# Kernel optimization log

Hardware: AMD Instinct MI355X
Metric: run time of the kernel (lower is better)

The kernel has to match this reference:

```python
import jax, jax.numpy as jnp
import numpy as np

D_MODEL = 1024
D_INNER = 2048   # expand * d_model
D_STATE = 16
D_CONV = 4
DT_RANK = 64     # ceil(d_model / 16)
BATCH = 4
SEQLEN = 2048


def _dw_causal_conv(x, w, b):
    # x: (B, d, L); w: (d, 1, K) depthwise; causal left pad K-1 -> output length L
    y = jax.lax.conv_general_dilated(
        x, w, window_strides=(1,), padding=[(D_CONV - 1, 0)],
        dimension_numbers=("NCH", "OIH", "NCH"), feature_group_count=x.shape[1])
    return y + b[None, :, None]


def _ssm_pass(x_conv, z, A_log, x_proj_w, dt_proj_w, dt_proj_b, D):
    # x_conv, z: (B, d, L)
    Bsz, d, L = x_conv.shape
    u = jax.nn.silu(x_conv)                                   # (B, d, L)
    x_dbl = jnp.einsum("bdl,rd->blr", u, x_proj_w)            # (B, L, dt_rank+2N)
    dt = x_dbl[..., :DT_RANK]
    Bm = x_dbl[..., DT_RANK:DT_RANK + D_STATE]                # (B, L, N)
    Cm = x_dbl[..., DT_RANK + D_STATE:]                       # (B, L, N)
    delta = jax.nn.softplus(jnp.einsum("blr,dr->bld", dt, dt_proj_w) + dt_proj_b)  # (B, L, d)
    A = -jnp.exp(A_log)                                       # (d, N)

    # time-major inputs for scan
    delta_t = jnp.transpose(delta, (1, 0, 2))                 # (L, B, d)
    u_t = jnp.transpose(u, (2, 0, 1))                         # (L, B, d)
    Bm_t = jnp.transpose(Bm, (1, 0, 2))                       # (L, B, N)
    Cm_t = jnp.transpose(Cm, (1, 0, 2))                       # (L, B, N)

    def step(h, inp):
        d_s, B_s, C_s, u_s = inp                              # (B,d) (B,N) (B,N) (B,d)
        dA = jnp.exp(d_s[:, :, None] * A)                     # (B, d, N)
        h = dA * h + (d_s * u_s)[:, :, None] * B_s[:, None, :]
        y = jnp.einsum("bdn,bn->bd", h, C_s)
        return h, y

    h0 = jnp.zeros((Bsz, d, D_STATE), dtype=u.dtype)
    _, ys = jax.lax.scan(step, h0, (delta_t, Bm_t, Cm_t, u_t))  # ys: (L, B, d)
    y = jnp.transpose(ys, (1, 2, 0)) + D[None, :, None] * u     # (B, d, L)
    return y * jax.nn.silu(z)


def setup_inputs() -> dict:
    key = jax.random.key(0)
    ks = jax.random.split(key, 16)
    s = 0.02
    hidden_states = jax.random.normal(ks[0], (BATCH, SEQLEN, D_MODEL), jnp.float32)
    in_proj_w = jax.random.normal(ks[1], (2 * D_INNER, D_MODEL), jnp.float32) * s
    conv_w_f = jax.random.normal(ks[2], (D_INNER, 1, D_CONV), jnp.float32) * 0.2
    conv_b_f = jax.random.normal(ks[3], (D_INNER,), jnp.float32) * 0.1
    conv_w_b = jax.random.normal(ks[4], (D_INNER, 1, D_CONV), jnp.float32) * 0.2
    conv_b_b = jax.random.normal(ks[5], (D_INNER,), jnp.float32) * 0.1
    x_proj_w_f = jax.random.normal(ks[6], (DT_RANK + 2 * D_STATE, D_INNER), jnp.float32) * s
    dt_proj_w_f = jax.random.uniform(ks[7], (D_INNER, DT_RANK), jnp.float32, -DT_RANK**-0.5, DT_RANK**-0.5)
    x_proj_w_b = jax.random.normal(ks[8], (DT_RANK + 2 * D_STATE, D_INNER), jnp.float32) * s
    dt_proj_w_b = jax.random.uniform(ks[9], (D_INNER, DT_RANK), jnp.float32, -DT_RANK**-0.5, DT_RANK**-0.5)
    # dt bias init: inverse-softplus of dt sampled log-uniform in [1e-3, 1e-1]
    dt = jnp.exp(jax.random.uniform(ks[10], (D_INNER,)) * (np.log(0.1) - np.log(0.001)) + np.log(0.001))
    dt = jnp.clip(dt, 1e-4, None)
    inv_dt = dt + jnp.log(-jnp.expm1(-dt))
    dt_proj_b_f = inv_dt
    dt_proj_b_b = inv_dt
    A_log = jnp.log(jnp.broadcast_to(jnp.arange(1, D_STATE + 1, dtype=jnp.float32), (D_INNER, D_STATE)))
    out_proj_w = jax.random.normal(ks[11], (D_MODEL, D_INNER), jnp.float32) * s
    return {
        "hidden_states": hidden_states, "in_proj_w": in_proj_w,
        "conv_w_f": conv_w_f, "conv_b_f": conv_b_f, "conv_w_b": conv_w_b, "conv_b_b": conv_b_b,
        "x_proj_w_f": x_proj_w_f, "dt_proj_w_f": dt_proj_w_f, "dt_proj_b_f": dt_proj_b_f,
        "x_proj_w_b": x_proj_w_b, "dt_proj_w_b": dt_proj_w_b, "dt_proj_b_b": dt_proj_b_b,
        "A_log_f": A_log, "A_log_b": A_log,
        "D_f": jnp.ones((D_INNER,), jnp.float32), "D_b": jnp.ones((D_INNER,), jnp.float32),
        "out_proj_w": out_proj_w,
    }


def reference(hidden_states, in_proj_w, conv_w_f, conv_b_f, conv_w_b, conv_b_b,
              x_proj_w_f, dt_proj_w_f, dt_proj_b_f, x_proj_w_b, dt_proj_w_b, dt_proj_b_b,
              A_log_f, A_log_b, D_f, D_b, out_proj_w):
    L = hidden_states.shape[1]
    xz = jnp.einsum("bld,ed->bel", hidden_states, in_proj_w)  # (B, 2*d_inner, L)
    x, z = xz[:, :D_INNER], xz[:, D_INNER:]

    # forward direction
    x_conv_f = _dw_causal_conv(x, conv_w_f, conv_b_f)[..., :L]
    y_f = _ssm_pass(x_conv_f, z, A_log_f, x_proj_w_f, dt_proj_w_f, dt_proj_b_f, D_f)

    # backward direction
    x_b, z_b = x[..., ::-1], z[..., ::-1]
    x_conv_b = _dw_causal_conv(x_b, conv_w_b, conv_b_b)[..., :L]
    y_b = _ssm_pass(x_conv_b, z_b, A_log_b, x_proj_w_b, dt_proj_w_b, dt_proj_b_b, D_b)[..., ::-1]

    y = (y_f + y_b) / 2.0                                     # if_divide_out=True
    out = jnp.einsum("bdl,ed->ble", y, out_proj_w)            # (B, L, d_model)
    return out
```

## Files before the change

### kernel.cpp

```cpp
#include <hip/hip_runtime.h>


#define Bsz  4
#define LSEQ 2048
#define DM   1024
#define DI   2048
#define DS   16
#define MROWS (Bsz * LSEQ)
#define NCH  32
#define CLEN 64

typedef unsigned short u16b;
typedef __attribute__((ext_vector_type(8))) short short8;
typedef __attribute__((ext_vector_type(4))) float f32x4;
typedef __attribute__((address_space(3))) unsigned int lds_u32;
typedef const __attribute__((address_space(1))) unsigned int glb_u32;

__device__ __forceinline__ float b2f(u16b u) {
  union { unsigned int i; float f; } x; x.i = ((unsigned int)u) << 16; return x.f;
}
__device__ __forceinline__ u16b f2b(float f) {
  union { float f; unsigned int i; } x; x.f = f;
  unsigned int r = x.i + 0x7FFFu + ((x.i >> 16) & 1u);
  return (u16b)(r >> 16);
}
__device__ __forceinline__ u16b f2b_cvt(float f) {
  unsigned int r;
  asm("v_cvt_pk_bf16_f32 %0, %1, %1" : "=v"(r) : "v"(f));
  return (u16b)r;
}
__device__ __forceinline__ float fast_rcp(float x) {
  return __builtin_amdgcn_rcpf(x);
}
__device__ __forceinline__ float softplus_fast(float v) {
  float e = __expf(-fabsf(v));
  return fmaxf(v, 0.f) + __logf(1.f + e);
}
__device__ __forceinline__ void pow_ladder(float q, float* dA) {
  float q2 = q * q, q3 = q2 * q, q4 = q2 * q2;
  float q5 = q4 * q, q6 = q4 * q2, q7 = q4 * q3, q8 = q4 * q4;
  dA[0] = q;  dA[1] = q2;  dA[2] = q3;  dA[3] = q4;
  dA[4] = q5; dA[5] = q6;  dA[6] = q7;  dA[7] = q8;
  dA[8] = q8 * q;  dA[9] = q8 * q2;  dA[10] = q8 * q3;  dA[11] = q8 * q4;
  dA[12] = q8 * q5; dA[13] = q8 * q6; dA[14] = q8 * q7; dA[15] = q8 * q8;
}

__device__ __forceinline__ int xcd_swz(int id, int nwg) {
  int c = nwg >> 3;
  return (id & 7) * c + (id >> 3);
}

__device__ __forceinline__ void stage_tile(const u16b* gbase, int ld,
                                           u16b* lds, int wave, int lane) {
#pragma unroll
  for (int t = 0; t < 4; ++t) {
    int rb = wave * 32 + t * 8;
    int r = rb + (lane >> 3);
    int cb = (lane & 7) ^ (r & 7);
    const u16b* g = gbase + (size_t)r * ld + cb * 8;
    __builtin_amdgcn_global_load_lds((glb_u32*)g, (lds_u32*)(lds + rb * 64),
                                     16, 0, 0);
  }
}

__global__ void sniff_kernel(const unsigned int* __restrict__ p,
                             int* __restrict__ flag) {
  unsigned int w = p[threadIdx.x];
  int e = (w >> 7) & 0xFF;
  unsigned long long m = __ballot(e >= 110 && e <= 135);
  if (threadIdx.x == 0) *flag = (__popcll(m) >= 32) ? 1 : 0;
}

__global__ __launch_bounds__(256) void convert_kernel(
    const void* __restrict__ src, u16b* __restrict__ dst, int n,
    const int* __restrict__ flag) {
  int i = (blockIdx.x * 256 + threadIdx.x) * 8;
  if (i >= n) return;
  if (*flag) {
    *(uint4*)(dst + i) = *(const uint4*)((const u16b*)src + i);
  } else {
    const float* s = (const float*)src;
    float4 a = *(const float4*)(s + i);
    float4 b = *(const float4*)(s + i + 4);
    u16b o[8] = {f2b(a.x), f2b(a.y), f2b(a.z), f2b(a.w),
                 f2b(b.x), f2b(b.y), f2b(b.z), f2b(b.w)};
    *(uint4*)(dst + i) = *(uint4*)o;
  }
}

struct SmallTab { const void* s[14]; u16b* d[14]; };
__global__ __launch_bounds__(256) void convert_small_kernel(
    SmallTab t, const int* __restrict__ flag) {
  const int pref[15] = {0,4,5,9,10,106,170,171,267,331,332,348,364,365,366};
  int bx = blockIdx.x;
  int seg = 0;
#pragma unroll
  for (int i = 0; i < 14; ++i)
    if (bx >= pref[i + 1]) seg = i + 1;
  int idx = (bx - pref[seg]) * 2048 + threadIdx.x * 8;
  u16b* dst = t.d[seg];
  if (*flag) {
    *(uint4*)(dst + idx) = *(const uint4*)((const u16b*)t.s[seg] + idx);
  } else {
    const float* s = (const float*)t.s[seg];
    float4 a = *(const float4*)(s + idx);
    float4 b = *(const float4*)(s + idx + 4);
    u16b o[8] = {f2b(a.x), f2b(a.y), f2b(a.z), f2b(a.w),
                 f2b(b.x), f2b(b.y), f2b(b.z), f2b(b.w)};
    *(uint4*)(dst + idx) = *(uint4*)o;
  }
}

#define BM 128
#define BN 128
#define BK 64

template<int EPI>
__global__ __launch_bounds__(256) void gemm_kernel(
    const u16b* __restrict__ A, const u16b* __restrict__ B, void* __restrict__ Cptr,
    const int* __restrict__ flag, int M, int N, int K, int lda, int ldb, int ldc) {
  __shared__ u16b As[BM * BK];
  __shared__ u16b Bs[BN * BK];
  const int tid = threadIdx.x;
  const int nbx = gridDim.x;
  const int id = xcd_swz(blockIdx.y * nbx + blockIdx.x, nbx * gridDim.y);
  const int n0 = (id % nbx) * BN;
  const int m0 = (id / nbx) * BM;
  const int wave = tid >> 6, lane = tid & 63;
  const int wm = (wave >> 1) * 64, wn = (wave & 1) * 64;
  const int lr = lane & 15, lg = lane >> 4;
  u16b* C = (u16b*)Cptr;
  float* Cf = (float*)Cptr;
  const int fl = (EPI == 3) ? flag[0] : 1;

  f32x4 acc[4][4] = {};

  for (int k0 = 0; k0 < K; k0 += BK) {
    stage_tile(A + (size_t)m0 * lda + k0, lda, As, wave, lane);
    stage_tile(B + (size_t)n0 * ldb + k0, ldb, Bs, wave, lane);
    __syncthreads();
#pragma unroll
    for (int kk = 0; kk < BK; kk += 32) {
      short8 afr[4], bfr[4];
#pragma unroll
      for (int i = 0; i < 4; ++i) {
        int r = wm + i * 16 + lr;
        afr[i] = *(const short8*)&As[r * 64 + (((kk >> 3) + lg) ^ (r & 7)) * 8];
      }
#pragma unroll
      for (int j = 0; j < 4; ++j) {
        int r = wn + j * 16 + lr;
        bfr[j] = *(const short8*)&Bs[r * 64 + (((kk >> 3) + lg) ^ (r & 7)) * 8];
      }
#pragma unroll
      for (int i = 0; i < 4; ++i)
#pragma unroll
        for (int j = 0; j < 4; ++j)
          acc[i][j] = __builtin_amdgcn_mfma_f32_16x16x32_bf16(
              afr[i], bfr[j], acc[i][j], 0, 0, 0);
    }
    __syncthreads();
  }

#pragma unroll
  for (int i = 0; i < 4; ++i) {
    int rbase = m0 + wm + i * 16 + lg * 4;
#pragma unroll
    for (int j = 0; j < 4; ++j) {
      int col = n0 + wn + j * 16 + lr;
      if (col < N) {
#pragma unroll
        for (int e = 0; e < 4; ++e) {
          float v = acc[i][j][e];
          size_t ci = (size_t)(rbase + e) * ldc + col;
          if (EPI == 3) {
            if (fl) C[ci] = f2b(v); else Cf[ci] = v;
          } else {
            C[ci] = f2b(v);
          }
        }
      }
    }
  }
}

template<int EPI>
__global__ __launch_bounds__(256) void gemm2_kernel(
    const u16b* __restrict__ A, const u16b* __restrict__ B1,
    const u16b* __restrict__ B2, u16b* __restrict__ C1, u16b* __restrict__ C2,
    const u16b* __restrict__ bias1, const u16b* __restrict__ bias2,
    float* __restrict__ aux1, float* __restrict__ aux2,
    int Mhalf, int N, int K, int lda, int ldb, int ldc1, int ldc2) {
  __shared__ u16b As[BM * BK];
  __shared__ u16b Bs[BN * BK];
  const int tid = threadIdx.x;
  const int nbx = gridDim.x;
  const int id = xcd_swz(blockIdx.y * nbx + blockIdx.x, nbx * gridDim.y);
  const int n0 = (id % nbx) * BN;
  const int m0 = (id / nbx) * BM;
  const int hi = (m0 >= Mhalf);
  const u16b* B = hi ? B2 : B1;
  u16b* C = hi ? C2 : C1;
  const u16b* bias = hi ? bias2 : bias1;
  float* aux = hi ? aux2 : aux1;
  const int ldc = hi ? ldc2 : ldc1;
  const int mloc = m0 - (hi ? Mhalf : 0);
  const int wave = tid >> 6, lane = tid & 63;
  const int wm = (wave >> 1) * 64, wn = (wave & 1) * 64;
  const int lr = lane & 15, lg = lane >> 4;

  f32x4 acc[4][4] = {};

  for (int k0 = 0; k0 < K; k0 += BK) {
    stage_tile(A + (size_t)m0 * lda + k0, lda, As, wave, lane);
    stage_tile(B + (size_t)n0 * ldb + k0, ldb, Bs, wave, lane);
    __syncthreads();
#pragma unroll
    for (int kk = 0; kk < BK; kk += 32) {
      short8 afr[4], bfr[4];
#pragma unroll
      for (int i = 0; i < 4; ++i) {
        int r = wm + i * 16 + lr;
        afr[i] = *(const short8*)&As[r * 64 + (((kk >> 3) + lg) ^ (r & 7)) * 8];
      }
#pragma unroll
      for (int j = 0; j < 4; ++j) {
        int r = wn + j * 16 + lr;
        bfr[j] = *(const short8*)&Bs[r * 64 + (((kk >> 3) + lg) ^ (r & 7)) * 8];
      }
#pragma unroll
      for (int i = 0; i < 4; ++i)
#pragma unroll
        for (int j = 0; j < 4; ++j)
          acc[i][j] = __builtin_amdgcn_mfma_f32_16x16x32_bf16(
              afr[i], bfr[j], acc[i][j], 0, 0, 0);
    }
    __syncthreads();
  }

#pragma unroll
  for (int i = 0; i < 4; ++i) {
    int rbase = mloc + wm + i * 16 + lg * 4;
#pragma unroll
    for (int j = 0; j < 4; ++j) {
      int col = n0 + wn + j * 16 + lr;
      if (col < N) {
        float bv = (EPI == 1) ? b2f(bias[col]) : 0.f;
#pragma unroll
        for (int e = 0; e < 4; ++e) {
          float v = acc[i][j][e];
          if (EPI == 1) v = softplus_fast(v + bv);
          C[(size_t)(rbase + e) * ldc + col] = f2b(v);
          if (EPI == 2 && col >= 64)
            aux[(size_t)(rbase + e) * 32 + (col - 64)] = v;
        }
      }
    }
  }
}

__global__ __launch_bounds__(256) void conv_kernel(
    const u16b* __restrict__ xz, const u16b* __restrict__ cwf,
    const u16b* __restrict__ cbf, const u16b* __restrict__ cwb,
    const u16b* __restrict__ cbb, u16b* __restrict__ u_f,
    u16b* __restrict__ u_b) {
  int gid = blockIdx.x * 256 + threadIdx.x;
  int d = gid & (DI - 1);
  int m = gid >> 11;
  int b = m >> 11;
  int l = m & (LSEQ - 1);
  const u16b* xcol = xz + ((size_t)b * LSEQ) * (2 * DI) + d;
  float xv[7];
#pragma unroll
  for (int t = 0; t < 7; ++t) {
    int ll = l + t - 3;
    xv[t] = (ll >= 0 && ll < LSEQ) ? b2f(xcol[(size_t)ll * (2 * DI)]) : 0.f;
  }
  float af = b2f(cbf[d]);
#pragma unroll
  for (int k = 0; k < 4; ++k) af = fmaf(b2f(cwf[d * 4 + k]), xv[k], af);
  float ab = b2f(cbb[d]);
#pragma unroll
  for (int j = 0; j < 4; ++j) ab = fmaf(b2f(cwb[d * 4 + 3 - j]), xv[3 + j], ab);
  float sf = af * fast_rcp(1.f + __expf(-af));
  float sb = ab * fast_rcp(1.f + __expf(-ab));
  u_f[(size_t)m * DI + d] = f2b(sf);
  u_b[((size_t)b * LSEQ + (LSEQ - 1 - l)) * DI + d] = f2b(sb);
}

__device__ __forceinline__ bool detect_intA(const u16b* alog, int d, float* An2) {
  bool fast = true;
#pragma unroll
  for (int n = 0; n < DS; ++n) {
    float a = __expf(b2f(alog[d * DS + n]));
    An2[n] = -a * 1.44269504088896f;
    fast = fast && (fabsf(a - (float)(n + 1)) < 0.02f * (float)(n + 1));
  }
  return fast;
}

#define CHUNK_BODY_FAST() do {                                        \
    float du = cd * cu; s += cd;                                      \
    float dA[DS]; pow_ladder(__expf(-cd), dA);                        \
    _Pragma("unroll") for (int n = 0; n < DS; ++n)                    \
      h[n] = fmaf(dA[n], h[n], du * bl[n]);                           \
    bl += 32;                                                         \
  } while (0)

#define CHUNK_BODY_SLOW() do {                                        \
    float du = cd * cu; s += cd;                                      \
    _Pragma("unroll") for (int n = 0; n < DS; ++n) {                  \
      float dA = exp2f(cd * An2[n]);                                  \
      h[n] = fmaf(dA, h[n], du * bl[n]);                              \
    }                                                                 \
    bl += 32;                                                         \
  } while (0)

__global__ __launch_bounds__(256) void scan_chunk_kernel(
    const u16b* __restrict__ xz, const u16b* __restrict__ u_f,
    const u16b* __restrict__ u_b, const u16b* __restrict__ dltb,
    const float* __restrict__ bc_f, const float* __restrict__ bc_b,
    const u16b* __restrict__ alog_f, const u16b* __restrict__ alog_b,
    float* __restrict__ hstate, float* __restrict__ sdelta) {
  __shared__ float bcs[CLEN * 32];
  int bx = blockIdx.x;
  int dblk = bx & 7;
  int chunk = (bx >> 3) & 31;
  int b = (bx >> 8) & 3;
  int dir = bx >> 10;
  int d = dblk * 256 + threadIdx.x;

  const u16b* uptr = dir ? u_b : u_f;
  const u16b* dlt = dir ? dltb : xz;
  const int ldd = dir ? DI : 2 * DI;
  const float* bcp = dir ? bc_b : bc_f;
  const u16b* alog = dir ? alog_b : alog_f;

  const size_t mb = (size_t)b * LSEQ + (size_t)chunk * CLEN;
  {
    const float* src = bcp + mb * 32;
    int t = threadIdx.x * 8;
    *(f32x4*)&bcs[t] = *(const f32x4*)&src[t];
    *(f32x4*)&bcs[t + 4] = *(const f32x4*)&src[t + 4];
  }
  float An2[DS];
  bool fastA = detect_intA(alog, d, An2);
  __syncthreads();

  float h[DS];
#pragma unroll
  for (int n = 0; n < DS; ++n) h[n] = 0.f;
  float s = 0.f;
  unsigned od = (unsigned)mb * (unsigned)ldd + (unsigned)d;
  unsigned ou = (unsigned)mb * DI + (unsigned)d;
  float nd = b2f(dlt[od]);
  float nu = b2f(uptr[ou]);
  const float* bl = bcs;
  float cd, cu;
  if (fastA) {
#pragma unroll 4
    for (int l = 0; l < CLEN - 1; ++l) {
      cd = nd; cu = nu;
      od += ldd; ou += DI;
      nd = b2f(dlt[od]); nu = b2f(uptr[ou]);
      CHUNK_BODY_FAST();
    }
    cd = nd; cu = nu;
    CHUNK_BODY_FAST();
  } else {
#pragma unroll 4
    for (int l = 0; l < CLEN - 1; ++l) {
      cd = nd; cu = nu;
      od += ldd; ou += DI;
      nd = b2f(dlt[od]); nu = b2f(uptr[ou]);
      CHUNK_BODY_SLOW();
    }
    cd = nd; cu = nu;
    CHUNK_BODY_SLOW();
  }
  size_t slot = (size_t)((dir * 4 + b) * 32 + chunk) * 2048 + d;
  float* hp = hstate + slot * 16;
#pragma unroll
  for (int i = 0; i < 4; ++i)
    ((f32x4*)hp)[i] = *(f32x4*)&h[i * 4];
  sdelta[slot] = s;
}

__global__ __launch_bounds__(256) void scan_carry_kernel(
    const u16b* __restrict__ alog_f, const u16b* __restrict__ alog_b,
    float* __restrict__ hstate, const float* __restrict__ sdelta) {
  int gid = blockIdx.x * 256 + threadIdx.x;
  int n = gid & (DS - 1);
  int d = (gid >> 4) & (DI - 1);
  int b = (gid >> 15) & 3;
  int dir = gid >> 17;
  const u16b* alog = dir ? alog_b : alog_f;
  float An2 = -__expf(b2f(alog[d * DS + n])) * 1.44269504088896f;
  float h = 0.f;
  size_t base = (size_t)((dir * 4 + b) * 32) * 2048 + d;
  for (int c = 0; c < NCH; ++c) {
    size_t slot = base + (size_t)c * 2048;
    float sdv = sdelta[slot];
    float* hp = hstate + slot * 16 + n;
    float hl = *hp;
    float P = exp2f(An2 * sdv);
    float nh = fmaf(P, h, hl);
    *hp = h;
    h = nh;
  }
}

#define APPLY_BODY_FAST() do {                                        \
    float du = cd * cu;                                               \
    float dA[DS]; pow_ladder(__expf(-cd), dA);                        \
    float y0 = 0.f, y1 = 0.f;                                         \
    _Pragma("unroll") for (int n = 0; n < DS; n += 2) {               \
      h[n] = fmaf(dA[n], h[n], du * bl[n]);                           \
      y0 = fmaf(h[n], bl[16 + n], y0);                                \
      h[n + 1] = fmaf(dA[n + 1], h[n + 1], du * bl[n + 1]);           \
      y1 = fmaf(h[n + 1], bl[17 + n], y1);                            \
    }                                                                 \
    float sz = cz * fast_rcp(1.f + __expf(-cz));                      \
    float out = (y0 + y1 + Dd * cu) * sz;                             \
    uptr[oo] = f2b_cvt(out); oo += DI; bl += 32;                      \
  } while (0)

#define APPLY_BODY_SLOW() do {                                        \
    float du = cd * cu;                                               \
    float y = 0.f;                                                    \
    _Pragma("unroll") for (int n = 0; n < DS; ++n) {                  \
      float dA = exp2f(cd * An2[n]);                                  \
      h[n] = fmaf(dA, h[n], du * bl[n]);                              \
      y = fmaf(h[n], bl[16 + n], y);                                  \
    }                                                                 \
    float sz = cz * fast_rcp(1.f + __expf(-cz));                      \
    float out = (y + Dd * cu) * sz;                                   \
    uptr[oo] = f2b_cvt(out); oo += DI; bl += 32;                      \
  } while (0)

__global__ __launch_bounds__(256) void scan_apply_kernel(
    const u16b* __restrict__ xz, u16b* __restrict__ u_f,
    u16b* __restrict__ u_b, const u16b* __restrict__ dltb,
    const float* __restrict__ bc_f, const float* __restrict__ bc_b,
    const u16b* __restrict__ alog_f, const u16b* __restrict__ alog_b,
    const u16b* __restrict__ dv_f, const u16b* __restrict__ dv_b,
    const float* __restrict__ hstate) {
  __shared__ float bcs[CLEN * 32];
  int bx = blockIdx.x;
  int dblk = bx & 7;
  int chunk = (bx >> 3) & 31;
  int b = (bx >> 8) & 3;
  int dir = bx >> 10;
  int d = dblk * 256 + threadIdx.x;

  u16b* uptr = dir ? u_b : u_f;
  const u16b* dlt = dir ? dltb : xz;
  const int ldd = dir ? DI : 2 * DI;
  const float* bcp = dir ? bc_b : bc_f;
  const u16b* alog = dir ? alog_b : alog_f;
  const u16b* dv = dir ? dv_b : dv_f;

  const size_t mb0 = (size_t)b * LSEQ;
  const size_t mb = mb0 + (size_t)chunk * CLEN;
  {
    const float* src = bcp + mb * 32;
    int t = threadIdx.x * 8;
    *(f32x4*)&bcs[t] = *(const f32x4*)&src[t];
    *(f32x4*)&bcs[t + 4] = *(const f32x4*)&src[t + 4];
  }
  float An2[DS];
  bool fastA = detect_intA(alog, d, An2);
  float Dd = b2f(dv[d]);
  float h[DS];
  {
    size_t slot = (size_t)((dir * 4 + b) * 32 + chunk) * 2048 + d;
    const float* hp = hstate + slot * 16;
#pragma unroll
    for (int i = 0; i < 4; ++i)
      *(f32x4*)&h[i * 4] = ((const f32x4*)hp)[i];
  }
  __syncthreads();

  size_t zs0 = dir ? (mb0 + (LSEQ - 1 - (size_t)chunk * CLEN)) : mb;
  const int zst = dir ? -(2 * DI) : (2 * DI);
  unsigned od = (unsigned)mb * (unsigned)ldd + (unsigned)d;
  unsigned ou = (unsigned)mb * DI + (unsigned)d;
  unsigned oo = ou;
  int oz = (int)zs0 * (2 * DI) + DI + d;
  float nd = b2f(dlt[od]);
  float nu = b2f(uptr[ou]);
  float nz = b2f(xz[oz]);
  const float* bl = bcs;
  float cd, cu, cz;
  if (fastA) {
#pragma unroll 4
    for (int l = 0; l < CLEN - 1; ++l) {
      cd = nd; cu = nu; cz = nz;
      od += ldd; ou += DI; oz += zst;
      nd = b2f(dlt[od]); nu = b2f(uptr[ou]); nz = b2f(xz[oz]);
      APPLY_BODY_FAST();
    }
    cd = nd; cu = nu; cz = nz;
    APPLY_BODY_FAST();
  } else {
#pragma unroll 4
    for (int l = 0; l < CLEN - 1; ++l) {
      cd = nd; cu = nu; cz = nz;
      od += ldd; ou += DI; oz += zst;
      nd = b2f(dlt[od]); nu = b2f(uptr[ou]); nz = b2f(xz[oz]);
      APPLY_BODY_SLOW();
    }
    cd = nd; cu = nu; cz = nz;
    APPLY_BODY_SLOW();
  }
}

__global__ __launch_bounds__(256) void combine_kernel(
    const u16b* __restrict__ yf, const u16b* __restrict__ yb_rev,
    u16b* __restrict__ yc) {
  size_t i = ((size_t)blockIdx.x * 256 + threadIdx.x) * 8;
  size_t m = i >> 11;
  size_t dcol = i & (DI - 1);
  size_t mr = m ^ (LSEQ - 1);
  uint4 a = *(const uint4*)(yf + m * DI + dcol);
  uint4 b = *(const uint4*)(yb_rev + mr * DI + dcol);
  const u16b* ap = (const u16b*)&a;
  const u16b* bp = (const u16b*)&b;
  uint4 o;
  u16b* op = (u16b*)&o;
#pragma unroll
  for (int j = 0; j < 8; ++j) op[j] = f2b(0.5f * (b2f(ap[j]) + b2f(bp[j])));
  *(uint4*)(yc + i) = o;
}

extern "C" void kernel_launch(void* const* d_in, const int* in_sizes, int n_in,
                              void* d_out, int out_size, void* d_ws,
                              size_t ws_size, hipStream_t stream) {
  char* ws = (char*)d_ws;
  u16b* xz    = (u16b*)(ws);
  u16b* u_f   = (u16b*)(ws + 67108864);
  u16b* u_b   = (u16b*)(ws + 100663296);
  u16b* arena = (u16b*)(ws + 134217728);
  u16b* xdf   = (u16b*)(ws + 167772160);
  u16b* xdb   = (u16b*)(ws + 169345024);
  float* bcf  = (float*)(ws + 170917888);
  float* bcb  = (float*)(ws + 171966464);
  u16b* opw_c  = (u16b*)(ws + 173015040);
  u16b* xpwf_c = (u16b*)(ws + 177209344);
  u16b* xpwb_c = (u16b*)(ws + 177602560);
  u16b* dpwf_c = (u16b*)(ws + 177995776);
  u16b* dpwb_c = (u16b*)(ws + 178257920);
  u16b* cwf_c  = (u16b*)(ws + 178520064);
  u16b* cwb_c  = (u16b*)(ws + 178536448);
  u16b* cbf_c  = (u16b*)(ws + 178552832);
  u16b* cbb_c  = (u16b*)(ws + 178556928);
  u16b* dpbf_c = (u16b*)(ws + 178561024);
  u16b* dpbb_c = (u16b*)(ws + 178565120);
  u16b* alf_c  = (u16b*)(ws + 178569216);
  u16b* alb_c  = (u16b*)(ws + 178634752);
  u16b* dvf_c  = (u16b*)(ws + 178700288);
  u16b* dvb_c  = (u16b*)(ws + 178704384);
  int*  flag   = (int*)(ws + 178708480);
  float* hstate = (float*)(ws + 178712576);
  float* sdelta = (float*)(ws + 212267008);

  u16b* hs_c  = arena;
  u16b* inw_c = arena + 8388608;
  u16b* dltb  = arena;
  u16b* y_c   = arena;

  dim3 blk(256);
  sniff_kernel<<<dim3(1), dim3(64), 0, stream>>>((const unsigned int*)d_in[0], flag);
  convert_kernel<<<dim3(4096), blk, 0, stream>>>(d_in[0], hs_c, 8388608, flag);
  convert_kernel<<<dim3(2048), blk, 0, stream>>>(d_in[1], inw_c, 4194304, flag);
  convert_kernel<<<dim3(1024), blk, 0, stream>>>(d_in[16], opw_c, 2097152, flag);
  SmallTab st = {{d_in[2], d_in[3], d_in[4], d_in[5], d_in[6], d_in[7], d_in[8],
                  d_in[9], d_in[10], d_in[11], d_in[12], d_in[13], d_in[14],
                  d_in[15]},
                 {cwf_c, cbf_c, cwb_c, cbb_c, xpwf_c, dpwf_c, dpbf_c, xpwb_c,
                  dpwb_c, dpbb_c, alf_c, alb_c, dvf_c, dvb_c}};
  convert_small_kernel<<<dim3(366), blk, 0, stream>>>(st, flag);

  gemm_kernel<0><<<dim3(32, 64), blk, 0, stream>>>(hs_c, inw_c, xz, flag,
      MROWS, 2 * DI, DM, DM, DM, 2 * DI);
  conv_kernel<<<dim3(65536), blk, 0, stream>>>(xz, cwf_c, cbf_c, cwb_c, cbb_c,
                                               u_f, u_b);
  gemm2_kernel<2><<<dim3(1, 128), blk, 0, stream>>>(u_f, xpwf_c, xpwb_c,
      xdf, xdb, nullptr, nullptr, bcf, bcb, MROWS, 96, DI, DI, DI, 96, 96);
  gemm2_kernel<1><<<dim3(16, 128), blk, 0, stream>>>(xdf, dpwf_c, dpwb_c,
      xz, dltb, dpbf_c, dpbb_c, nullptr, nullptr, MROWS, DI, 64, 96, 64,
      2 * DI, DI);
  scan_chunk_kernel<<<dim3(2048), blk, 0, stream>>>(xz, u_f, u_b, dltb, bcf,
      bcb, alf_c, alb_c, hstate, sdelta);
  scan_carry_kernel<<<dim3(1024), blk, 0, stream>>>(alf_c, alb_c, hstate, sdelta);
  scan_apply_kernel<<<dim3(2048), blk, 0, stream>>>(xz, u_f, u_b, dltb, bcf,
      bcb, alf_c, alb_c, dvf_c, dvb_c, hstate);
  combine_kernel<<<dim3(8192), blk, 0, stream>>>(u_f, u_b, y_c);
  gemm_kernel<3><<<dim3(8, 64), blk, 0, stream>>>(y_c, opw_c, d_out, flag,
      MROWS, DM, DI, DI, DI, DM);
}
```

Baseline: 561.7 us.

## Split-K the x_proj GEMM with a reduce pass and read B/C from global memory

The x_proj GEMM (N=96, K=2048) launched only 128 blocks. It is replaced by a split-K version with two K halves writing fp32 partials, plus a separate reduce kernel that sums them and writes the bf16 x_dbl and fp32 B/C buffers. Separately, the scan chunk and apply kernels drop their LDS staging of B/C and the barrier, reading B/C straight from global memory, which should hit in cache. This adds a partial buffer round trip and an extra launch. It may also slow the scan loops if the global reads are not served from cache.

```diff
diff --git a/kernel.cpp b/kernel.cpp
--- a/kernel.cpp
+++ b/kernel.cpp
@@ -259,6 +259,84 @@
   }
 }
 
+__global__ __launch_bounds__(256) void gemm2s_kernel(
+    const u16b* __restrict__ A, const u16b* __restrict__ B1,
+    const u16b* __restrict__ B2, float* __restrict__ P,
+    int Mhalf, int Ksplit, int lda, int ldb) {
+  __shared__ u16b As[BM * BK];
+  __shared__ u16b Bs[BN * BK];
+  const int tid = threadIdx.x;
+  const int ks = blockIdx.x;
+  const int m0 = blockIdx.y * BM;
+  const int hi = (m0 >= Mhalf);
+  const u16b* B = hi ? B2 : B1;
+  const int wave = tid >> 6, lane = tid & 63;
+  const int wm = (wave >> 1) * 64, wn = (wave & 1) * 64;
+  const int lr = lane & 15, lg = lane >> 4;
+
+  f32x4 acc[4][4] = {};
+
+  const int kbeg = ks * Ksplit;
+  for (int k0 = kbeg; k0 < kbeg + Ksplit; k0 += BK) {
+    stage_tile(A + (size_t)m0 * lda + k0, lda, As, wave, lane);
+    stage_tile(B + k0, ldb, Bs, wave, lane);
+    __syncthreads();
+#pragma unroll
+    for (int kk = 0; kk < BK; kk += 32) {
+      short8 afr[4], bfr[4];
+#pragma unroll
+      for (int i = 0; i < 4; ++i) {
+        int r = wm + i * 16 + lr;
+        afr[i] = *(const short8*)&As[r * 64 + (((kk >> 3) + lg) ^ (r & 7)) * 8];
+      }
+#pragma unroll
+      for (int j = 0; j < 4; ++j) {
+        int r = wn + j * 16 + lr;
+        bfr[j] = *(const short8*)&Bs[r * 64 + (((kk >> 3) + lg) ^ (r & 7)) * 8];
+      }
+#pragma unroll
+      for (int i = 0; i < 4; ++i)
+#pragma unroll
+        for (int j = 0; j < 4; ++j)
+          acc[i][j] = __builtin_amdgcn_mfma_f32_16x16x32_bf16(
+              afr[i], bfr[j], acc[i][j], 0, 0, 0);
+    }
+    __syncthreads();
+  }
+
+  float* Pk = P + (size_t)ks * ((size_t)2 * Mhalf) * 128;
+#pragma unroll
+  for (int i = 0; i < 4; ++i) {
+    int rg = m0 + wm + i * 16 + lg * 4;
+#pragma unroll
+    for (int j = 0; j < 4; ++j) {
+      int col = wn + j * 16 + lr;
+#pragma unroll
+      for (int e = 0; e < 4; ++e)
+        Pk[(size_t)(rg + e) * 128 + col] = acc[i][j][e];
+    }
+  }
+}
+
+__global__ __launch_bounds__(256) void xdbl_reduce_kernel(
+    const float* __restrict__ P, u16b* __restrict__ xdf,
+    u16b* __restrict__ xdb, float* __restrict__ bcf,
+    float* __restrict__ bcb) {
+  int e = blockIdx.x * 256 + threadIdx.x;
+  int col = e & 127;
+  int m = e >> 7;
+  if (col >= 96) return;
+  float v = P[(size_t)e] + P[(size_t)e + (size_t)16384 * 128];
+  int hi = (m >= MROWS);
+  int mloc = m - (hi ? MROWS : 0);
+  u16b* C = hi ? xdb : xdf;
+  C[(size_t)mloc * 96 + col] = f2b(v);
+  if (col >= 64) {
+    float* aux = hi ? bcb : bcf;
+    aux[(size_t)mloc * 32 + (col - 64)] = v;
+  }
+}
+
 __global__ __launch_bounds__(256) void conv_kernel(
     const u16b* __restrict__ xz, const u16b* __restrict__ cwf,
     const u16b* __restrict__ cbf, const u16b* __restrict__ cwb,
@@ -322,7 +400,6 @@
     const float* __restrict__ bc_f, const float* __restrict__ bc_b,
     const u16b* __restrict__ alog_f, const u16b* __restrict__ alog_b,
     float* __restrict__ hstate, float* __restrict__ sdelta) {
-  __shared__ float bcs[CLEN * 32];
   int bx = blockIdx.x;
   int dblk = bx & 7;
   int chunk = (bx >> 3) & 31;
@@ -337,15 +414,9 @@
   const u16b* alog = dir ? alog_b : alog_f;
 
   const size_t mb = (size_t)b * LSEQ + (size_t)chunk * CLEN;
-  {
-    const float* src = bcp + mb * 32;
-    int t = threadIdx.x * 8;
-    *(f32x4*)&bcs[t] = *(const f32x4*)&src[t];
-    *(f32x4*)&bcs[t + 4] = *(const f32x4*)&src[t + 4];
-  }
+  const float* bl = bcp + mb * 32;
   float An2[DS];
   bool fastA = detect_intA(alog, d, An2);
-  __syncthreads();
 
   float h[DS];
 #pragma unroll
@@ -355,7 +426,6 @@
   unsigned ou = (unsigned)mb * DI + (unsigned)d;
   float nd = b2f(dlt[od]);
   float nu = b2f(uptr[ou]);
-  const float* bl = bcs;
   float cd, cu;
   if (fastA) {
 #pragma unroll 4
@@ -445,7 +515,6 @@
     const u16b* __restrict__ alog_f, const u16b* __restrict__ alog_b,
     const u16b* __restrict__ dv_f, const u16b* __restrict__ dv_b,
     const float* __restrict__ hstate) {
-  __shared__ float bcs[CLEN * 32];
   int bx = blockIdx.x;
   int dblk = bx & 7;
   int chunk = (bx >> 3) & 31;
@@ -462,12 +531,7 @@
 
   const size_t mb0 = (size_t)b * LSEQ;
   const size_t mb = mb0 + (size_t)chunk * CLEN;
-  {
-    const float* src = bcp + mb * 32;
-    int t = threadIdx.x * 8;
-    *(f32x4*)&bcs[t] = *(const f32x4*)&src[t];
-    *(f32x4*)&bcs[t + 4] = *(const f32x4*)&src[t + 4];
-  }
+  const float* bl = bcp + mb * 32;
   float An2[DS];
   bool fastA = detect_intA(alog, d, An2);
   float Dd = b2f(dv[d]);
@@ -479,7 +543,6 @@
     for (int i = 0; i < 4; ++i)
       *(f32x4*)&h[i * 4] = ((const f32x4*)hp)[i];
   }
-  __syncthreads();
 
   size_t zs0 = dir ? (mb0 + (LSEQ - 1 - (size_t)chunk * CLEN)) : mb;
   const int zst = dir ? -(2 * DI) : (2 * DI);
@@ -490,7 +553,6 @@
   float nd = b2f(dlt[od]);
   float nu = b2f(uptr[ou]);
   float nz = b2f(xz[oz]);
-  const float* bl = bcs;
   float cd, cu, cz;
   if (fastA) {
 #pragma unroll 4
@@ -566,6 +628,7 @@
 
   u16b* hs_c  = arena;
   u16b* inw_c = arena + 8388608;
+  float* Pbuf = (float*)arena;
   u16b* dltb  = arena;
   u16b* y_c   = arena;
 
@@ -585,8 +648,9 @@
       MROWS, 2 * DI, DM, DM, DM, 2 * DI);
   conv_kernel<<<dim3(65536), blk, 0, stream>>>(xz, cwf_c, cbf_c, cwb_c, cbb_c,
                                                u_f, u_b);
-  gemm2_kernel<2><<<dim3(1, 128), blk, 0, stream>>>(u_f, xpwf_c, xpwb_c,
-      xdf, xdb, nullptr, nullptr, bcf, bcb, MROWS, 96, DI, DI, DI, 96, 96);
+  gemm2s_kernel<<<dim3(2, 128), blk, 0, stream>>>(u_f, xpwf_c, xpwb_c, Pbuf,
+      MROWS, 1024, DI, DI);
+  xdbl_reduce_kernel<<<dim3(8192), blk, 0, stream>>>(Pbuf, xdf, xdb, bcf, bcb);
   gemm2_kernel<1><<<dim3(16, 128), blk, 0, stream>>>(xdf, dpwf_c, dpwb_c,
       xz, dltb, dpbf_c, dpbb_c, nullptr, nullptr, MROWS, DI, 64, 96, 64,
       2 * DI, DI);
```

New measurement: 550.3 us. 1.02x faster.
